# Kernel optimization log

Measured on AMD Instinct MI355X. Metric: run time of the kernel, lower is better.

The kernel has to match this reference:

```python
import jax, jax.numpy as jnp
import numpy as np

L, D, H, FF = 4, 256, 8, 1024
B, S = 4, 1024
HD = D // H
EPS = 1e-5


def layer_norm(x, g, b):
    mu = jnp.mean(x, axis=-1, keepdims=True)
    var = jnp.mean(jnp.square(x - mu), axis=-1, keepdims=True)
    return (x - mu) * jax.lax.rsqrt(var + EPS) * g + b


def setup_inputs() -> dict:
    key = jax.random.key(0)
    ks = jax.random.split(key, 16)
    sd = 0.02
    return {
        "x": jax.random.normal(ks[0], (B, S, D), dtype=jnp.float32),
        "mask": jnp.ones((B, S), dtype=jnp.int32),
        # per-layer stacked params (leading dim L); Linear stored as (in, out)
        "qkv_w": jax.random.normal(ks[1], (L, D, 3 * D), dtype=jnp.float32) * sd,
        "qkv_b": jnp.zeros((L, 3 * D), dtype=jnp.float32),
        "fc_w": jax.random.normal(ks[2], (L, D, D), dtype=jnp.float32) * sd,
        "fc_b": jnp.zeros((L, D), dtype=jnp.float32),
        "ln1_g": jnp.ones((L, D), dtype=jnp.float32),
        "ln1_b": jnp.zeros((L, D), dtype=jnp.float32),
        "ln2_g": jnp.ones((L, D), dtype=jnp.float32),
        "ln2_b": jnp.zeros((L, D), dtype=jnp.float32),
        "ff1_w": jax.random.normal(ks[3], (L, D, FF), dtype=jnp.float32) * sd,
        "ff1_b": jnp.zeros((L, FF), dtype=jnp.float32),
        "ff2_w": jax.random.normal(ks[4], (L, FF, D), dtype=jnp.float32) * sd,
        "ff2_b": jnp.zeros((L, D), dtype=jnp.float32),
    }


def reference(x, mask, qkv_w, qkv_b, fc_w, fc_b, ln1_g, ln1_b, ln2_g, ln2_b,
              ff1_w, ff1_b, ff2_w, ff2_b):
    # mask: 1 = valid token, 0 = pad
    neg_inf = jnp.finfo(x.dtype).min
    key_mask = (mask == 0)[:, None, None, :]  # [B,1,1,S]
    for l in range(L):
        residual = x
        qkv = x @ qkv_w[l] + qkv_b[l]                       # [B,S,3D]
        q, k, v = jnp.split(qkv, 3, axis=-1)
        q = q.reshape(B, S, H, HD).transpose(0, 2, 1, 3)    # [B,H,S,hd]
        k = k.reshape(B, S, H, HD).transpose(0, 2, 1, 3)
        v = v.reshape(B, S, H, HD).transpose(0, 2, 1, 3)
        attn = jnp.einsum('bhqd,bhkd->bhqk', q, k)          # scale=1 (scale=False)
        attn = jnp.where(key_mask, neg_inf, attn)
        attn = jax.nn.softmax(attn, axis=-1)
        o = jnp.einsum('bhqk,bhkd->bhqd', attn, v)
        o = o.transpose(0, 2, 1, 3).reshape(B, S, D)
        o = o @ fc_w[l] + fc_b[l]
        x = layer_norm(o + residual, ln1_g[l], ln1_b[l])    # after_norm=True
        residual = x
        h = jax.nn.relu(x @ ff1_w[l] + ff1_b[l])
        h = h @ ff2_w[l] + ff2_b[l]
        x = layer_norm(residual + h, ln2_g[l], ln2_b[l])
    return x
```

## Files before the change

kernel.cpp:

```cpp
#include <hip/hip_runtime.h>
#include <hip/hip_bf16.h>
#include <math.h>

#define NL 4
#define DMODEL 256
#define NH 8
#define FFDIM 1024
#define BB 4
#define SS 1024
#define HDIM 32
#define MROWS (BB * SS)
#define LN_EPS 1e-5f

typedef __bf16 bf16x8 __attribute__((ext_vector_type(8)));
typedef float f32x4 __attribute__((ext_vector_type(4)));
typedef short s16x4 __attribute__((ext_vector_type(4)));
typedef unsigned int u32;

__device__ __forceinline__ ushort f2bf(float f) {
    uint u = __builtin_bit_cast(uint, f);
    u += 0x7fff + ((u >> 16) & 1);
    return (ushort)(u >> 16);
}
__device__ __forceinline__ uint pack2(float a, float b) {
    return (uint)f2bf(a) | ((uint)f2bf(b) << 16);
}

__device__ __forceinline__ int xcd_swz(int bid, int nwg) {
    return (bid & 7) * (nwg >> 3) + (bid >> 3);
}

template<int N> __device__ __forceinline__ void vmcnt_wait() {
    asm volatile("s_waitcnt vmcnt(%0)" :: "n"(N) : "memory");
}
__device__ __forceinline__ void raw_barrier() {
    asm volatile("s_barrier" ::: "memory");
}

__device__ __forceinline__ void async_ld16(const void* g, void* l) {
    __builtin_amdgcn_global_load_lds(
        (const __attribute__((address_space(1))) u32*)g,
        (__attribute__((address_space(3))) u32*)l, 16, 0, 0);
}

#if __has_builtin(__builtin_amdgcn_ds_read_tr16_b64)
#define TR_BUILTIN 1
#else
#define TR_BUILTIN 0
#endif

__device__ __forceinline__ s16x4 tr16(const ushort* p) {
    __attribute__((address_space(3))) s16x4* ap =
        (__attribute__((address_space(3))) s16x4*)p;
#if TR_BUILTIN
    return __builtin_amdgcn_ds_read_tr16_b64(ap);
#else
    s16x4 r;
    asm volatile("ds_read_b64_tr_b16 %0, %1" : "=v"(r) : "v"(ap) : "memory");
    return r;
#endif
}
__device__ __forceinline__ void tr_fence() {
#if !TR_BUILTIN
    asm volatile("s_waitcnt lgkmcnt(0)" ::: "memory");
    __builtin_amdgcn_sched_barrier(0);
#endif
}

__global__ __launch_bounds__(256)
void wconv_all(const float* __restrict__ qkv_w, const float* __restrict__ fc_w,
               const float* __restrict__ ff1_w, const float* __restrict__ ff2_w,
               ushort* __restrict__ wq, ushort* __restrict__ wfc,
               ushort* __restrict__ wf1, ushort* __restrict__ wf2)
{
    const int l = blockIdx.z;
    int t = blockIdx.x;
    const float* src; ushort* dst; int K, N, nx;
    if (t < 192)      {          src = qkv_w; dst = wq;  K = 256;  N = 768;  nx = 24; }
    else if (t < 256) { t -= 192; src = fc_w;  dst = wfc; K = 256;  N = 256;  nx = 8; }
    else if (t < 512) { t -= 256; src = ff1_w; dst = wf1; K = 256;  N = 1024; nx = 32; }
    else              { t -= 512; src = ff2_w; dst = wf2; K = 1024; N = 256;  nx = 8; }
    src += (size_t)l * K * N;
    dst += (size_t)l * K * N;
    const int n0 = (t % nx) * 32, k0 = (t / nx) * 32;

    __shared__ ushort tt[32][33];
    const int tn = threadIdx.x & 31, tk8 = threadIdx.x >> 5;
    #pragma unroll
    for (int i = 0; i < 4; ++i)
        tt[tn][tk8 + i * 8] = f2bf(src[(size_t)(k0 + tk8 + i * 8) * N + n0 + tn]);
    __syncthreads();
    #pragma unroll
    for (int i = 0; i < 4; ++i)
        dst[(size_t)(n0 + tk8 + i * 8) * K + k0 + tn] = tt[tk8 + i * 8][tn];
}

__global__ __launch_bounds__(256)
void convert_x(const float* __restrict__ xin, float* __restrict__ x,
               ushort* __restrict__ xb)
{
    const size_t i = ((size_t)blockIdx.x * 256 + threadIdx.x) * 4;
    const float4 v = *reinterpret_cast<const float4*>(xin + i);
    *reinterpret_cast<float4*>(x + i) = v;
    uint2 p = make_uint2(pack2(v.x, v.y), pack2(v.z, v.w));
    *reinterpret_cast<uint2*>(xb + i) = p;
}

template<int BM, int BN, int WM, int WN, int ACT, int OBF>
__global__ __launch_bounds__(256)
void gemm_mfma(const ushort* __restrict__ A, const ushort* __restrict__ WT,
               const float* __restrict__ bias, float* __restrict__ Cf,
               ushort* __restrict__ Cb, int N, int K)
{
    constexpr int BK = 64;
    constexpr int WR = BM / WM;
    constexpr int WC = BN / WN;
    constexpr int MR = WR / 16, NR = WC / 16;
    constexpr int LSTG = BM / 32 + BN / 32;
    __shared__ __align__(16) ushort As[2][BM * BK];
    __shared__ __align__(16) ushort Bs[2][BN * BK];

    const int tid = threadIdx.x;
    const int lin = blockIdx.y * gridDim.x + blockIdx.x;
    const int work = xcd_swz(lin, gridDim.x * gridDim.y);
    const int m0 = (work / gridDim.x) * BM, n0 = (work % gridDim.x) * BN;
    const int wid = tid >> 6, lane = tid & 63;
    const int g = lane >> 4, c = lane & 15;
    const int wr = wid / WN, wc = wid % WN;

    auto stage = [&](int buf, int k0) {
        #pragma unroll
        for (int it = 0; it < (BM * BK * 2) / 4096; ++it) {
            const int o = tid * 16 + it * 4096;
            const int r = o >> 7;
            const int cb = (o & 127) ^ ((r & 7) << 4);
            async_ld16(A + (size_t)(m0 + r) * K + k0 + (cb >> 1),
                       (char*)&As[buf][0] + o);
        }
        #pragma unroll
        for (int it = 0; it < (BN * BK * 2) / 4096; ++it) {
            const int o = tid * 16 + it * 4096;
            const int r = o >> 7;
            const int cb = (o & 127) ^ ((r & 7) << 4);
            async_ld16(WT + (size_t)(n0 + r) * K + k0 + (cb >> 1),
                       (char*)&Bs[buf][0] + o);
        }
    };

    f32x4 acc[MR][NR] = {};

    stage(0, 0);

    int cur = 0;
    for (int k0 = 0; k0 < K; k0 += BK, cur ^= 1) {
        if (k0 + BK < K) { stage(cur ^ 1, k0 + BK); vmcnt_wait<LSTG>(); }
        else             { vmcnt_wait<0>(); }
        raw_barrier();

        #pragma unroll
        for (int ks = 0; ks < 2; ++ks) {
            bf16x8 af[MR], bfr[NR];
            #pragma unroll
            for (int mi = 0; mi < MR; ++mi) {
                const int row = wr * WR + mi * 16 + c;
                af[mi] = *(const bf16x8*)((const char*)&As[cur][0]
                    + row * 128 + ((ks * 64 + g * 16) ^ ((row & 7) << 4)));
            }
            #pragma unroll
            for (int ni = 0; ni < NR; ++ni) {
                const int row = wc * WC + ni * 16 + c;
                bfr[ni] = *(const bf16x8*)((const char*)&Bs[cur][0]
                    + row * 128 + ((ks * 64 + g * 16) ^ ((row & 7) << 4)));
            }
            #pragma unroll
            for (int mi = 0; mi < MR; ++mi)
                #pragma unroll
                for (int ni = 0; ni < NR; ++ni)
                    acc[mi][ni] = __builtin_amdgcn_mfma_f32_16x16x32_bf16(
                        af[mi], bfr[ni], acc[mi][ni], 0, 0, 0);
        }
        raw_barrier();
    }

    float bv[NR];
    #pragma unroll
    for (int ni = 0; ni < NR; ++ni)
        bv[ni] = bias[n0 + wc * WC + ni * 16 + c];

    #pragma unroll
    for (int mi = 0; mi < MR; ++mi) {
        #pragma unroll
        for (int j = 0; j < 4; ++j) {
            const int row = m0 + wr * WR + mi * 16 + g * 4 + j;
            #pragma unroll
            for (int ni = 0; ni < NR; ++ni) {
                float v = acc[mi][ni][j] + bv[ni];
                if (ACT) v = fmaxf(v, 0.f);
                const int col = n0 + wc * WC + ni * 16 + c;
                if (OBF) Cb[(size_t)row * N + col] = f2bf(v);
                else     Cf[(size_t)row * N + col] = v;
            }
        }
    }
}

template<int K>
__global__ __launch_bounds__(256)
void rowgemm_ln(const ushort* __restrict__ A, const ushort* __restrict__ WT,
                const float* __restrict__ bias, const float* __restrict__ lg,
                const float* __restrict__ lb, float* __restrict__ x,
                ushort* __restrict__ xb)
{
    constexpr int BK = 64, N = 256;
    __shared__ __align__(16) ushort As[2][16 * BK];
    __shared__ __align__(16) ushort Bs[2][N * BK];
    __shared__ float rsum[4][16], rsq[4][16], mval[16], ival[16];

    const int tid = threadIdx.x;
    const int m0 = blockIdx.x * 16;
    const int wid = tid >> 6, lane = tid & 63;
    const int g = lane >> 4, c = lane & 15;

    auto stage = [&](int buf, int k0) {
        if (tid < 128) {
            const int o = tid * 16;
            const int r = o >> 7;
            const int cb = (o & 127) ^ ((r & 7) << 4);
            async_ld16(A + (size_t)(m0 + r) * K + k0 + (cb >> 1),
                       (char*)&As[buf][0] + o);
        }
        #pragma unroll
        for (int it = 0; it < 8; ++it) {
            const int o = tid * 16 + it * 4096;
            const int r = o >> 7;
            const int cb = (o & 127) ^ ((r & 7) << 4);
            async_ld16(WT + (size_t)r * K + k0 + (cb >> 1),
                       (char*)&Bs[buf][0] + o);
        }
    };

    f32x4 acc[4] = {};

    stage(0, 0);

    int cur = 0;
    for (int k0 = 0; k0 < K; k0 += BK, cur ^= 1) {
        if (k0 + BK < K) {
            stage(cur ^ 1, k0 + BK);
            if (tid < 128) vmcnt_wait<9>(); else vmcnt_wait<8>();
        } else {
            vmcnt_wait<0>();
        }
        raw_barrier();

        #pragma unroll
        for (int ks = 0; ks < 2; ++ks) {
            const bf16x8 af = *(const bf16x8*)((const char*)&As[cur][0]
                + c * 128 + ((ks * 64 + g * 16) ^ ((c & 7) << 4)));
            #pragma unroll
            for (int ni = 0; ni < 4; ++ni) {
                const int row = wid * 64 + ni * 16 + c;
                const bf16x8 bf = *(const bf16x8*)((const char*)&Bs[cur][0]
                    + row * 128 + ((ks * 64 + g * 16) ^ ((row & 7) << 4)));
                acc[ni] = __builtin_amdgcn_mfma_f32_16x16x32_bf16(af, bf, acc[ni], 0, 0, 0);
            }
        }
        raw_barrier();
    }

    float bv[4], glv[4], blv[4];
    #pragma unroll
    for (int ni = 0; ni < 4; ++ni) {
        const int col = wid * 64 + ni * 16 + c;
        bv[ni] = bias[col]; glv[ni] = lg[col]; blv[ni] = lb[col];
    }

    #pragma unroll
    for (int j = 0; j < 4; ++j) {
        const int row = g * 4 + j;
        float s = 0.f;
        #pragma unroll
        for (int ni = 0; ni < 4; ++ni) {
            const int col = wid * 64 + ni * 16 + c;
            float vv = acc[ni][j] + bv[ni] + x[(size_t)(m0 + row) * N + col];
            acc[ni][j] = vv;
            s += vv;
        }
        #pragma unroll
        for (int off = 1; off < 16; off <<= 1) s += __shfl_xor(s, off);
        if (c == 0) rsum[wid][row] = s;
    }
    __syncthreads();
    if (tid < 16)
        mval[tid] = (rsum[0][tid] + rsum[1][tid] + rsum[2][tid] + rsum[3][tid])
                    * (1.f / N);
    __syncthreads();

    #pragma unroll
    for (int j = 0; j < 4; ++j) {
        const int row = g * 4 + j;
        const float mean = mval[row];
        float q = 0.f;
        #pragma unroll
        for (int ni = 0; ni < 4; ++ni) {
            const float d = acc[ni][j] - mean;
            q += d * d;
        }
        #pragma unroll
        for (int off = 1; off < 16; off <<= 1) q += __shfl_xor(q, off);
        if (c == 0) rsq[wid][row] = q;
    }
    __syncthreads();
    if (tid < 16) {
        const float q = rsq[0][tid] + rsq[1][tid] + rsq[2][tid] + rsq[3][tid];
        ival[tid] = rsqrtf(q * (1.f / N) + LN_EPS);
    }
    __syncthreads();

    #pragma unroll
    for (int j = 0; j < 4; ++j) {
        const int row = g * 4 + j;
        const float mean = mval[row], inv = ival[row];
        #pragma unroll
        for (int ni = 0; ni < 4; ++ni) {
            const int col = wid * 64 + ni * 16 + c;
            const float y = (acc[ni][j] - mean) * inv * glv[ni] + blv[ni];
            x[(size_t)(m0 + row) * N + col] = y;
            xb[(size_t)(m0 + row) * N + col] = f2bf(y);
        }
    }
}

__global__ __launch_bounds__(512)
void attn_mfma8(const ushort* __restrict__ qkv, const int* __restrict__ mask,
                ushort* __restrict__ out)
{
    const int tid = threadIdx.x;
    const int lane = tid & 63, wid = tid >> 6;
    const int g = lane >> 4, c = lane & 15;
    const int work = xcd_swz(blockIdx.x, 256);
    const int qblk = work & 7;
    const int bh = work >> 3;
    const int h = bh & (NH - 1), b = bh >> 3;
    const int q0 = qblk * 128 + wid * 16;

    __shared__ __align__(16) ushort Kb[2][128 * 32];
    __shared__ __align__(16) ushort Vs[2][2][128][16];
    __shared__ __align__(16) ushort Pl[8][16][136];
    __shared__ __align__(16) float  sbias[SS];
    __shared__ int mflag[8];

    const ushort* base  = qkv + (size_t)b * SS * 768;
    const ushort* kbase = base + DMODEL + h * HDIM;
    const ushort* vbase = base + 2 * DMODEL + h * HDIM;

    {
        const int i = tid * 2;
        const int2 mv = *reinterpret_cast<const int2*>(mask + b * SS + i);
        float2 bv;
        bv.x = mv.x ? 0.f : -3.4e38f;
        bv.y = mv.y ? 0.f : -3.4e38f;
        *reinterpret_cast<float2*>(&sbias[i]) = bv;
        const int miss = __any(!(mv.x && mv.y));
        if (lane == 0) mflag[wid] = miss;
    }

    const bf16x8 qfrag = *(const bf16x8*)(
        base + (size_t)(q0 + c) * 768 + h * HDIM + g * 8);

    const int o16   = tid * 16;
    const int krow  = o16 >> 6;
    const int kin   = (o16 & 63) ^ ((krow & 3) << 4);
    const int vhalf = o16 >> 12;
    const int vkey  = (o16 & 4095) >> 5;
    const int vd    = vhalf * 16 + (((o16 >> 4) & 1) << 3);

    #define STAGE(buf, koff)                                                   \
        do {                                                                   \
            async_ld16(kbase + (size_t)((koff) + krow) * 768 + (kin >> 1),     \
                       (char*)&Kb[buf][0] + o16);                              \
            async_ld16(vbase + (size_t)((koff) + vkey) * 768 + vd,             \
                       (char*)&Vs[buf][0][0][0] + o16);                        \
        } while (0)

    STAGE(0, 0);
    asm volatile("s_waitcnt lgkmcnt(0)" ::: "memory");
    raw_barrier();
    const int anyMasked = mflag[0] | mflag[1] | mflag[2] | mflag[3]
                        | mflag[4] | mflag[5] | mflag[6] | mflag[7];

    float m = -1e30f, lpart = 0.f;
    f32x4 o0 = {0.f, 0.f, 0.f, 0.f}, o1 = {0.f, 0.f, 0.f, 0.f};
    const f32x4 zf = {0.f, 0.f, 0.f, 0.f};

    for (int t = 0; t < 8; ++t) {
        const int cur = t & 1;
        if (t < 7) { STAGE(cur ^ 1, (t + 1) * 128); vmcnt_wait<2>(); }
        else       { vmcnt_wait<0>(); }
        raw_barrier();

        f32x4 s[8];
        __builtin_amdgcn_s_setprio(1);
        #pragma unroll
        for (int kt = 0; kt < 8; ++kt) {
            const int row = kt * 16 + c;
            const bf16x8 kf = *(const bf16x8*)((const char*)&Kb[cur][0]
                + row * 64 + ((g * 16) ^ ((c & 3) << 4)));
            s[kt] = __builtin_amdgcn_mfma_f32_16x16x32_bf16(kf, qfrag, zf, 0, 0, 0);
        }
        __builtin_amdgcn_s_setprio(0);

        if (anyMasked) {
            #pragma unroll
            for (int kt = 0; kt < 8; ++kt) {
                const f32x4 bv = *reinterpret_cast<const f32x4*>(
                    &sbias[t * 128 + kt * 16 + g * 4]);
                #pragma unroll
                for (int r = 0; r < 4; ++r) s[kt][r] += bv[r];
            }
        }

        union UU { s16x4 h[2]; bf16x8 v; };
        UU u0[4], u1[4];
        #pragma unroll
        for (int ks = 0; ks < 4; ++ks) {
            const int vr0 = ks * 32 + g * 8;
            u0[ks].h[0] = tr16(&Vs[cur][0][vr0][c]);
            u0[ks].h[1] = tr16(&Vs[cur][0][vr0 + 4][c]);
            u1[ks].h[0] = tr16(&Vs[cur][1][vr0][c]);
            u1[ks].h[1] = tr16(&Vs[cur][1][vr0 + 4][c]);
        }

        float mx = fmaxf(fmaxf(s[0][0], s[0][1]), fmaxf(s[0][2], s[0][3]));
        #pragma unroll
        for (int kt = 1; kt < 8; ++kt)
            mx = fmaxf(mx, fmaxf(fmaxf(s[kt][0], s[kt][1]),
                                 fmaxf(s[kt][2], s[kt][3])));
        if (!__all(mx <= m + 8.f)) {
            float fm = fmaxf(mx, __shfl_xor(mx, 16));
            fm = fmaxf(fm, __shfl_xor(fm, 32));
            const float mn = fmaxf(m, fm);
            const float sc = __expf(m - mn);
            m = mn;
            lpart *= sc;
            float scr[4];
            #pragma unroll
            for (int r = 0; r < 4; ++r) scr[r] = __shfl(sc, g * 4 + r);
            #pragma unroll
            for (int r = 0; r < 4; ++r) { o0[r] *= scr[r]; o1[r] *= scr[r]; }
        }

        float ls = 0.f;
        #pragma unroll
        for (int kt = 0; kt < 8; ++kt) {
            const float p0 = __expf(s[kt][0] - m);
            const float p1 = __expf(s[kt][1] - m);
            const float p2 = __expf(s[kt][2] - m);
            const float p3 = __expf(s[kt][3] - m);
            ls += (p0 + p1) + (p2 + p3);
            uint2 pk2 = make_uint2(pack2(p0, p1), pack2(p2, p3));
            *reinterpret_cast<uint2*>(&Pl[wid][c][kt * 16 + g * 4]) = pk2;
        }
        lpart += ls;

        tr_fence();
        __builtin_amdgcn_s_setprio(1);
        #pragma unroll
        for (int ks = 0; ks < 4; ++ks) {
            const bf16x8 pa = *(const bf16x8*)&Pl[wid][c][ks * 32 + g * 8];
            o0 = __builtin_amdgcn_mfma_f32_16x16x32_bf16(pa, u0[ks].v, o0, 0, 0, 0);
            o1 = __builtin_amdgcn_mfma_f32_16x16x32_bf16(pa, u1[ks].v, o1, 0, 0, 0);
        }
        __builtin_amdgcn_s_setprio(0);
        raw_barrier();
    }
    #undef STAGE

    float lsum = lpart;
    lsum += __shfl_xor(lsum, 16);
    lsum += __shfl_xor(lsum, 32);
    const float rs = 1.f / lsum;
    float inv[4];
    #pragma unroll
    for (int r = 0; r < 4; ++r) inv[r] = __shfl(rs, g * 4 + r);
    #pragma unroll
    for (int r = 0; r < 4; ++r) {
        ushort* op = out + (size_t)(b * SS + q0 + g * 4 + r) * DMODEL + h * HDIM;
        op[c]      = f2bf(o0[r] * inv[r]);
        op[16 + c] = f2bf(o1[r] * inv[r]);
    }
}

extern "C" void kernel_launch(void* const* d_in, const int* in_sizes, int n_in,
                              void* d_out, int out_size, void* d_ws, size_t ws_size,
                              hipStream_t stream)
{
    const float* x_in   = (const float*)d_in[0];
    const int*   maskp  = (const int*)d_in[1];
    const float* qkv_w  = (const float*)d_in[2];
    const float* qkv_b  = (const float*)d_in[3];
    const float* fc_w   = (const float*)d_in[4];
    const float* fc_b   = (const float*)d_in[5];
    const float* ln1_g  = (const float*)d_in[6];
    const float* ln1_b  = (const float*)d_in[7];
    const float* ln2_g  = (const float*)d_in[8];
    const float* ln2_b  = (const float*)d_in[9];
    const float* ff1_w  = (const float*)d_in[10];
    const float* ff1_b  = (const float*)d_in[11];
    const float* ff2_w  = (const float*)d_in[12];
    const float* ff2_b  = (const float*)d_in[13];

    float* x = (float*)d_out;

    ushort* wt_qkv = (ushort*)d_ws;
    ushort* wt_fc  = wt_qkv + (size_t)NL * 768 * 256;
    ushort* wt_ff1 = wt_fc  + (size_t)NL * 256 * 256;
    ushort* wt_ff2 = wt_ff1 + (size_t)NL * 1024 * 256;
    ushort* big    = wt_ff2 + (size_t)NL * 256 * 1024;
    ushort* attn_bf= big + (size_t)MROWS * FFDIM;
    ushort* x_bf   = attn_bf + (size_t)MROWS * DMODEL;

    wconv_all<<<dim3(768, 1, NL), 256, 0, stream>>>(
        qkv_w, fc_w, ff1_w, ff2_w, wt_qkv, wt_fc, wt_ff1, wt_ff2);
    convert_x<<<dim3(MROWS * DMODEL / 1024), 256, 0, stream>>>(x_in, x, x_bf);

    for (int l = 0; l < NL; ++l) {
        gemm_mfma<64, 64, 2, 2, 0, 1><<<dim3(12, 64), 256, 0, stream>>>(
            x_bf, wt_qkv + (size_t)l * 768 * 256, qkv_b + l * 768,
            nullptr, big, 768, 256);
        attn_mfma8<<<dim3(256), 512, 0, stream>>>(big, maskp, attn_bf);
        rowgemm_ln<256><<<dim3(256), 256, 0, stream>>>(
            attn_bf, wt_fc + (size_t)l * 256 * 256, fc_b + l * 256,
            ln1_g + l * DMODEL, ln1_b + l * DMODEL, x, x_bf);
        gemm_mfma<128, 64, 2, 2, 1, 1><<<dim3(16, 32), 256, 0, stream>>>(
            x_bf, wt_ff1 + (size_t)l * 1024 * 256, ff1_b + l * FFDIM,
            nullptr, big, 1024, 256);
        rowgemm_ln<1024><<<dim3(256), 256, 0, stream>>>(
            big, wt_ff2 + (size_t)l * 256 * 1024, ff2_b + l * DMODEL,
            ln2_g + l * DMODEL, ln2_b + l * DMODEL, x, x_bf);
    }
}
```

Before: 253.3 us.

## Fuse fc+LN1, FF1 with ReLU, and FF2+LN2 into one row-block kernel

Replaces three per-layer launches (fc projection with LN1, FF1 GEMM, FF2 with LN2) with a single kernel. Each block owns 16 rows and keeps the LN1 output and the 1024-wide ReLU hidden activations in shared memory, streaming all weight tiles through a double-buffered pipeline. This removes the global-memory round trip of the hidden activations and two launches. In exchange, every one of the 256 blocks re-reads the full FF1 and FF2 weights, shared memory use grows to about 108 KB per block (limiting occupancy), and FF1 now runs on a narrow 16-row tile instead of a wider GEMM tiling.

```diff
diff --git a/kernel.cpp b/kernel.cpp
--- a/kernel.cpp
+++ b/kernel.cpp
@@ -35,6 +35,9 @@
 }
 __device__ __forceinline__ void raw_barrier() {
     asm volatile("s_barrier" ::: "memory");
+}
+__device__ __forceinline__ void lgkm0() {
+    asm volatile("s_waitcnt lgkmcnt(0)" ::: "memory");
 }
 
 __device__ __forceinline__ void async_ld16(const void* g, void* l) {
@@ -204,16 +207,19 @@
     }
 }
 
-template<int K>
 __global__ __launch_bounds__(256)
-void rowgemm_ln(const ushort* __restrict__ A, const ushort* __restrict__ WT,
-                const float* __restrict__ bias, const float* __restrict__ lg,
-                const float* __restrict__ lb, float* __restrict__ x,
-                ushort* __restrict__ xb)
+void mlp_fused(const ushort* __restrict__ Aattn, const ushort* __restrict__ Wfc,
+               const float* __restrict__ bfc, const float* __restrict__ g1,
+               const float* __restrict__ be1, const ushort* __restrict__ W1,
+               const float* __restrict__ b1, const ushort* __restrict__ W2,
+               const float* __restrict__ b2, const float* __restrict__ g2,
+               const float* __restrict__ be2, float* __restrict__ x,
+               ushort* __restrict__ xb)
 {
-    constexpr int BK = 64, N = 256;
-    __shared__ __align__(16) ushort As[2][16 * BK];
-    __shared__ __align__(16) ushort Bs[2][N * BK];
+    __shared__ __align__(16) ushort As[2][16 * 64];
+    __shared__ __align__(16) ushort Bs[2][256 * 64];
+    __shared__ __align__(16) ushort ybf[16 * 256];
+    __shared__ __align__(16) ushort hbuf[16 * 1024];
     __shared__ float rsum[4][16], rsq[4][16], mval[16], ival[16];
 
     const int tid = threadIdx.x;
@@ -221,38 +227,41 @@
     const int wid = tid >> 6, lane = tid & 63;
     const int g = lane >> 4, c = lane & 15;
 
-    auto stage = [&](int buf, int k0) {
+    auto stageB = [&](int buf, const ushort* src, int ldk) {
+        #pragma unroll
+        for (int it = 0; it < 8; ++it) {
+            const int o = tid * 16 + it * 4096;
+            const int r = o >> 7;
+            const int cb = (o & 127) ^ ((r & 7) << 4);
+            async_ld16(src + (size_t)r * ldk + (cb >> 1), (char*)&Bs[buf][0] + o);
+        }
+    };
+    auto stageA = [&](int buf, int k0) {
         if (tid < 128) {
             const int o = tid * 16;
             const int r = o >> 7;
             const int cb = (o & 127) ^ ((r & 7) << 4);
-            async_ld16(A + (size_t)(m0 + r) * K + k0 + (cb >> 1),
+            async_ld16(Aattn + (size_t)(m0 + r) * 256 + k0 + (cb >> 1),
                        (char*)&As[buf][0] + o);
         }
-        #pragma unroll
-        for (int it = 0; it < 8; ++it) {
-            const int o = tid * 16 + it * 4096;
-            const int r = o >> 7;
-            const int cb = (o & 127) ^ ((r & 7) << 4);
-            async_ld16(WT + (size_t)r * K + k0 + (cb >> 1),
-                       (char*)&Bs[buf][0] + o);
-        }
     };
 
     f32x4 acc[4] = {};
-
-    stage(0, 0);
-
+    const f32x4 zf = {0.f, 0.f, 0.f, 0.f};
+
+    stageA(0, 0); stageB(0, Wfc, 256);
     int cur = 0;
-    for (int k0 = 0; k0 < K; k0 += BK, cur ^= 1) {
-        if (k0 + BK < K) {
-            stage(cur ^ 1, k0 + BK);
+    #pragma unroll
+    for (int k = 0; k < 4; ++k, cur ^= 1) {
+        if (k < 3) {
+            stageA(cur ^ 1, (k + 1) * 64);
+            stageB(cur ^ 1, Wfc + (k + 1) * 64, 256);
             if (tid < 128) vmcnt_wait<9>(); else vmcnt_wait<8>();
         } else {
-            vmcnt_wait<0>();
-        }
-        raw_barrier();
-
+            stageB(cur ^ 1, W1, 256);
+            vmcnt_wait<8>();
+        }
+        raw_barrier();
         #pragma unroll
         for (int ks = 0; ks < 2; ++ks) {
             const bf16x8 af = *(const bf16x8*)((const char*)&As[cur][0]
@@ -268,65 +277,195 @@
         raw_barrier();
     }
 
-    float bv[4], glv[4], blv[4];
-    #pragma unroll
-    for (int ni = 0; ni < 4; ++ni) {
-        const int col = wid * 64 + ni * 16 + c;
-        bv[ni] = bias[col]; glv[ni] = lg[col]; blv[ni] = lb[col];
-    }
-
-    #pragma unroll
-    for (int j = 0; j < 4; ++j) {
-        const int row = g * 4 + j;
-        float s = 0.f;
+    float res[4][4];
+    {
+        float bv[4], gl[4], bl[4];
         #pragma unroll
         for (int ni = 0; ni < 4; ++ni) {
             const int col = wid * 64 + ni * 16 + c;
-            float vv = acc[ni][j] + bv[ni] + x[(size_t)(m0 + row) * N + col];
-            acc[ni][j] = vv;
-            s += vv;
-        }
-        #pragma unroll
-        for (int off = 1; off < 16; off <<= 1) s += __shfl_xor(s, off);
-        if (c == 0) rsum[wid][row] = s;
-    }
-    __syncthreads();
-    if (tid < 16)
-        mval[tid] = (rsum[0][tid] + rsum[1][tid] + rsum[2][tid] + rsum[3][tid])
-                    * (1.f / N);
-    __syncthreads();
-
-    #pragma unroll
-    for (int j = 0; j < 4; ++j) {
-        const int row = g * 4 + j;
-        const float mean = mval[row];
-        float q = 0.f;
-        #pragma unroll
-        for (int ni = 0; ni < 4; ++ni) {
-            const float d = acc[ni][j] - mean;
-            q += d * d;
-        }
-        #pragma unroll
-        for (int off = 1; off < 16; off <<= 1) q += __shfl_xor(q, off);
-        if (c == 0) rsq[wid][row] = q;
-    }
-    __syncthreads();
-    if (tid < 16) {
-        const float q = rsq[0][tid] + rsq[1][tid] + rsq[2][tid] + rsq[3][tid];
-        ival[tid] = rsqrtf(q * (1.f / N) + LN_EPS);
-    }
-    __syncthreads();
-
-    #pragma unroll
-    for (int j = 0; j < 4; ++j) {
-        const int row = g * 4 + j;
-        const float mean = mval[row], inv = ival[row];
+            bv[ni] = bfc[col]; gl[ni] = g1[col]; bl[ni] = be1[col];
+        }
+        #pragma unroll
+        for (int j = 0; j < 4; ++j) {
+            const int row = g * 4 + j;
+            float s = 0.f;
+            #pragma unroll
+            for (int ni = 0; ni < 4; ++ni) {
+                const int col = wid * 64 + ni * 16 + c;
+                float vv = acc[ni][j] + bv[ni] + x[(size_t)(m0 + row) * 256 + col];
+                acc[ni][j] = vv;
+                s += vv;
+            }
+            #pragma unroll
+            for (int off = 1; off < 16; off <<= 1) s += __shfl_xor(s, off);
+            if (c == 0) rsum[wid][row] = s;
+        }
+        __syncthreads();
+        if (tid < 16)
+            mval[tid] = (rsum[0][tid] + rsum[1][tid] + rsum[2][tid] + rsum[3][tid])
+                        * (1.f / 256);
+        __syncthreads();
+        #pragma unroll
+        for (int j = 0; j < 4; ++j) {
+            const int row = g * 4 + j;
+            const float mean = mval[row];
+            float q = 0.f;
+            #pragma unroll
+            for (int ni = 0; ni < 4; ++ni) {
+                const float d = acc[ni][j] - mean;
+                q += d * d;
+            }
+            #pragma unroll
+            for (int off = 1; off < 16; off <<= 1) q += __shfl_xor(q, off);
+            if (c == 0) rsq[wid][row] = q;
+        }
+        __syncthreads();
+        if (tid < 16) {
+            const float q = rsq[0][tid] + rsq[1][tid] + rsq[2][tid] + rsq[3][tid];
+            ival[tid] = rsqrtf(q * (1.f / 256) + LN_EPS);
+        }
+        __syncthreads();
+        #pragma unroll
+        for (int j = 0; j < 4; ++j) {
+            const int row = g * 4 + j;
+            const float mean = mval[row], inv = ival[row];
+            #pragma unroll
+            for (int ni = 0; ni < 4; ++ni) {
+                const int col = wid * 64 + ni * 16 + c;
+                const float y = (acc[ni][j] - mean) * inv * gl[ni] + bl[ni];
+                res[ni][j] = y;
+                const int byteo = row * 512 + ((col * 2) ^ ((row & 7) << 4));
+                *(ushort*)((char*)ybf + byteo) = f2bf(y);
+                acc[ni][j] = 0.f;
+            }
+        }
+    }
+    lgkm0();
+    raw_barrier();
+
+    #pragma unroll 1
+    for (int s = 0; s < 16; ++s, cur ^= 1) {
+        const int kk = s & 3;
+        if (s < 15) {
+            const int s2 = s + 1;
+            stageB(cur ^ 1, W1 + (size_t)((s2 >> 2) * 256) * 256 + (s2 & 3) * 64, 256);
+            vmcnt_wait<8>();
+        } else {
+            stageB(cur ^ 1, W2, 1024);
+            vmcnt_wait<8>();
+        }
+        raw_barrier();
+        #pragma unroll
+        for (int ks = 0; ks < 2; ++ks) {
+            const int kbyte = (kk * 64 + ks * 32 + g * 8) * 2;
+            const bf16x8 af = *(const bf16x8*)((const char*)ybf
+                + c * 512 + (kbyte ^ ((c & 7) << 4)));
+            #pragma unroll
+            for (int ni = 0; ni < 4; ++ni) {
+                const int row = wid * 64 + ni * 16 + c;
+                const bf16x8 bf = *(const bf16x8*)((const char*)&Bs[cur][0]
+                    + row * 128 + ((ks * 64 + g * 16) ^ ((row & 7) << 4)));
+                acc[ni] = __builtin_amdgcn_mfma_f32_16x16x32_bf16(af, bf, acc[ni], 0, 0, 0);
+            }
+        }
+        raw_barrier();
+        if (kk == 3) {
+            const int nt = s >> 2;
+            #pragma unroll
+            for (int j = 0; j < 4; ++j) {
+                const int row = g * 4 + j;
+                #pragma unroll
+                for (int ni = 0; ni < 4; ++ni) {
+                    const int col = nt * 256 + wid * 64 + ni * 16 + c;
+                    const float h = fmaxf(acc[ni][j] + b1[col], 0.f);
+                    const int byteo = row * 2048 + ((col * 2) ^ ((row & 7) << 4));
+                    *(ushort*)((char*)hbuf + byteo) = f2bf(h);
+                    acc[ni][j] = 0.f;
+                }
+            }
+        }
+    }
+    lgkm0();
+    raw_barrier();
+
+    #pragma unroll 1
+    for (int s = 0; s < 16; ++s, cur ^= 1) {
+        if (s < 15) { stageB(cur ^ 1, W2 + (s + 1) * 64, 1024); vmcnt_wait<8>(); }
+        else        { vmcnt_wait<0>(); }
+        raw_barrier();
+        #pragma unroll
+        for (int ks = 0; ks < 2; ++ks) {
+            const int kbyte = (s * 64 + ks * 32 + g * 8) * 2;
+            const bf16x8 af = *(const bf16x8*)((const char*)hbuf
+                + c * 2048 + (kbyte ^ ((c & 7) << 4)));
+            #pragma unroll
+            for (int ni = 0; ni < 4; ++ni) {
+                const int row = wid * 64 + ni * 16 + c;
+                const bf16x8 bf = *(const bf16x8*)((const char*)&Bs[cur][0]
+                    + row * 128 + ((ks * 64 + g * 16) ^ ((row & 7) << 4)));
+                acc[ni] = __builtin_amdgcn_mfma_f32_16x16x32_bf16(af, bf, acc[ni], 0, 0, 0);
+            }
+        }
+        raw_barrier();
+    }
+
+    {
+        float bv[4], gl[4], bl[4];
         #pragma unroll
         for (int ni = 0; ni < 4; ++ni) {
             const int col = wid * 64 + ni * 16 + c;
-            const float y = (acc[ni][j] - mean) * inv * glv[ni] + blv[ni];
-            x[(size_t)(m0 + row) * N + col] = y;
-            xb[(size_t)(m0 + row) * N + col] = f2bf(y);
+            bv[ni] = b2[col]; gl[ni] = g2[col]; bl[ni] = be2[col];
+        }
+        #pragma unroll
+        for (int j = 0; j < 4; ++j) {
+            const int row = g * 4 + j;
+            float s = 0.f;
+            #pragma unroll
+            for (int ni = 0; ni < 4; ++ni) {
+                float vv = acc[ni][j] + bv[ni] + res[ni][j];
+                acc[ni][j] = vv;
+                s += vv;
+            }
+            #pragma unroll
+            for (int off = 1; off < 16; off <<= 1) s += __shfl_xor(s, off);
+            if (c == 0) rsum[wid][row] = s;
+        }
+        __syncthreads();
+        if (tid < 16)
+            mval[tid] = (rsum[0][tid] + rsum[1][tid] + rsum[2][tid] + rsum[3][tid])
+                        * (1.f / 256);
+        __syncthreads();
+        #pragma unroll
+        for (int j = 0; j < 4; ++j) {
+            const int row = g * 4 + j;
+            const float mean = mval[row];
+            float q = 0.f;
+            #pragma unroll
+            for (int ni = 0; ni < 4; ++ni) {
+                const float d = acc[ni][j] - mean;
+                q += d * d;
+            }
+            #pragma unroll
+            for (int off = 1; off < 16; off <<= 1) q += __shfl_xor(q, off);
+            if (c == 0) rsq[wid][row] = q;
+        }
+        __syncthreads();
+        if (tid < 16) {
+            const float q = rsq[0][tid] + rsq[1][tid] + rsq[2][tid] + rsq[3][tid];
+            ival[tid] = rsqrtf(q * (1.f / 256) + LN_EPS);
+        }
+        __syncthreads();
+        #pragma unroll
+        for (int j = 0; j < 4; ++j) {
+            const int row = g * 4 + j;
+            const float mean = mval[row], inv = ival[row];
+            #pragma unroll
+            for (int ni = 0; ni < 4; ++ni) {
+                const int col = wid * 64 + ni * 16 + c;
+                const float y = (acc[ni][j] - mean) * inv * gl[ni] + bl[ni];
+                x[(size_t)(m0 + row) * 256 + col] = y;
+                xb[(size_t)(m0 + row) * 256 + col] = f2bf(y);
+            }
         }
     }
 }
@@ -384,7 +523,7 @@
         } while (0)
 
     STAGE(0, 0);
-    asm volatile("s_waitcnt lgkmcnt(0)" ::: "memory");
+    lgkm0();
     raw_barrier();
     const int anyMasked = mflag[0] | mflag[1] | mflag[2] | mflag[3]
                         | mflag[4] | mflag[5] | mflag[6] | mflag[7];
@@ -529,14 +668,11 @@
             x_bf, wt_qkv + (size_t)l * 768 * 256, qkv_b + l * 768,
             nullptr, big, 768, 256);
         attn_mfma8<<<dim3(256), 512, 0, stream>>>(big, maskp, attn_bf);
-        rowgemm_ln<256><<<dim3(256), 256, 0, stream>>>(
+        mlp_fused<<<dim3(256), 256, 0, stream>>>(
             attn_bf, wt_fc + (size_t)l * 256 * 256, fc_b + l * 256,
-            ln1_g + l * DMODEL, ln1_b + l * DMODEL, x, x_bf);
-        gemm_mfma<128, 64, 2, 2, 1, 1><<<dim3(16, 32), 256, 0, stream>>>(
-            x_bf, wt_ff1 + (size_t)l * 1024 * 256, ff1_b + l * FFDIM,
-            nullptr, big, 1024, 256);
-        rowgemm_ln<1024><<<dim3(256), 256, 0, stream>>>(
-            big, wt_ff2 + (size_t)l * 256 * 1024, ff2_b + l * DMODEL,
+            ln1_g + l * DMODEL, ln1_b + l * DMODEL,
+            wt_ff1 + (size_t)l * 1024 * 256, ff1_b + l * FFDIM,
+            wt_ff2 + (size_t)l * 256 * 1024, ff2_b + l * DMODEL,
             ln2_g + l * DMODEL, ln2_b + l * DMODEL, x, x_bf);
     }
 }
```

New measurement: 222.5 us. -12.2%, faster.
